# Performance work log

Hardware: AMD Instinct MI355X
Metric: run time of the kernel (lower is better)

Reference implementation:

```python
import jax, jax.numpy as jnp
import numpy as np

CONTACT_THRESH = 0.01
COLLISION_THRESH = 0.005
WEIGHT_PEN = 100.0
WEIGHT_MISS = 10.0
# MANO fingertip + palm contact-zone vertex indices (hardcoded in module)
CONTACT_IDX = np.array([745, 317, 444, 556, 673, 95, 182, 234, 279, 320])

SCALE = 0.1  # place points in a 0.1 m cube so mm-scale thresholds are meaningful


def setup_inputs() -> dict:
    key = jax.random.key(0)
    k1, k2, k3, k4 = jax.random.split(key, 4)
    B, NH, V = 8, 778, 40000
    hand_verts = jax.random.uniform(k1, (B, NH, 3), dtype=jnp.float32) * SCALE
    obj_verts = jax.random.uniform(k2, (B, V, 3), dtype=jnp.float32) * SCALE
    hand_faces = jax.random.randint(k3, (1538, 3), 0, NH, dtype=jnp.int64 if jax.config.read('jax_enable_x64') else jnp.int32)
    obj_faces = jax.random.randint(k4, (79996, 3), 0, V, dtype=jnp.int64 if jax.config.read('jax_enable_x64') else jnp.int32)
    return {"hand_verts": hand_verts, "obj_verts": obj_verts,
            "hand_faces": hand_faces, "obj_faces": obj_faces}


def _min_dists(a, b):
    """Brute-force 1-NN: min Euclidean distance from each point in a [B,N,3] to b [B,M,3] -> [B,N]."""
    a_sq = jnp.sum(a * a, axis=-1, keepdims=True)          # [B,N,1]
    b_sq = jnp.sum(b * b, axis=-1)                          # [B,M]
    ab = jnp.einsum('bnd,bmd->bnm', a, b)                   # [B,N,M]
    d2 = jnp.maximum(a_sq + b_sq[:, None, :] - 2.0 * ab, 0.0)
    return jnp.sqrt(jnp.min(d2, axis=2))                    # [B,N]


def _masked_mean(vals, mask):
    cnt = jnp.sum(mask)
    s = jnp.sum(jnp.where(mask, vals, 0.0))
    return jnp.where(cnt > 0, s / jnp.maximum(cnt, 1).astype(vals.dtype), jnp.zeros((), vals.dtype))


def reference(hand_verts, obj_verts, hand_faces, obj_faces):
    # faces are unused by the loss (as in the torch module)
    idx = jnp.asarray(CONTACT_IDX)
    # distances are computed under no_grad / detached in the original
    dists = jax.lax.stop_gradient(_min_dists(hand_verts, obj_verts))              # [B,778]
    contact_dists = jax.lax.stop_gradient(_min_dists(hand_verts[:, idx, :], obj_verts))  # [B,10]

    pen_mask = dists < COLLISION_THRESH
    pen_loss = _masked_mean((COLLISION_THRESH - dists) ** 2, pen_mask)

    att_mask = (contact_dists > COLLISION_THRESH) & (contact_dists < CONTACT_THRESH)
    att_loss = _masked_mean(contact_dists ** 2, att_mask)

    contact_loss = WEIGHT_PEN * pen_loss + WEIGHT_MISS * att_loss
    dist_mean = jnp.mean(dists)
    num_contacts = jnp.sum(att_mask).astype(jnp.int32)
    num_penetrations = jnp.sum(pen_mask).astype(jnp.int32)
    return (contact_loss, pen_loss, att_loss, dist_mean, num_contacts, num_penetrations)
```

## Files before the change

### kernel.cpp

```cpp
#include <hip/hip_runtime.h>
#include <math.h>

constexpr int NH    = 778;
constexpr int GRIDC = 16;
constexpr int NCELL = GRIDC * GRIDC * GRIDC;
constexpr int CAP   = 40;
constexpr float CELL     = 0.1f / GRIDC;
constexpr float INV_CELL = GRIDC / 0.1f;
constexpr int NXCD = 8;


__device__ __forceinline__ int clampc(int v) {
    return min(GRIDC - 1, max(0, v));
}

__global__ __launch_bounds__(256) void bin_kernel(
    const float* __restrict__ obj,
    int* __restrict__ cnt,
    int* __restrict__ ocnt,
    float4* __restrict__ buckets,
    float4* __restrict__ ovf,
    int B, int V, int bpb)
{
    const int w = (blockIdx.x % NXCD) * (gridDim.x / NXCD) + blockIdx.x / NXCD;
    const int b = w / bpb;
    const int p = (w % bpb) * 256 + threadIdx.x;
    if (b >= B || p >= V) return;
    const int i = b * V + p;

    const float x = obj[3 * i + 0];
    const float y = obj[3 * i + 1];
    const float z = obj[3 * i + 2];
    const int cx = clampc((int)(x * INV_CELL));
    const int cy = clampc((int)(y * INV_CELL));
    const int cz = clampc((int)(z * INV_CELL));
    const int cell = b * NCELL + (cz * GRIDC + cy) * GRIDC + cx;
    const int idx = atomicAdd(&cnt[cell], 1);
    if (idx < CAP) {
        buckets[(size_t)cell * CAP + idx] = make_float4(x, y, z, 0.f);
    } else {
        const int oi = atomicAdd(ocnt, 1);
        ovf[oi] = make_float4(x, y, z, __int_as_float(b));
    }
}

__global__ __launch_bounds__(256) void query_kernel(
    const float* __restrict__ hand,
    const int* __restrict__ cnt,
    const float4* __restrict__ buckets,
    const float4* __restrict__ ovf,
    const int* __restrict__ ocnt,
    float* __restrict__ dist,
    int B, int bpq)
{
    const int tid  = threadIdx.x;
    const int wave = tid >> 6;
    const int lane = tid & 63;
    const int w = (blockIdx.x % NXCD) * (gridDim.x / NXCD) + blockIdx.x / NXCD;
    const int b  = w / bpq;
    const int ql = (w % bpq) * 4 + wave;
    if (b >= B || ql >= NH) return;
    const int i = b * NH + ql;

    const float hx = hand[3 * i + 0];
    const float hy = hand[3 * i + 1];
    const float hz = hand[3 * i + 2];
    const int hcx = clampc((int)(hx * INV_CELL));
    const int hcy = clampc((int)(hy * INV_CELL));
    const int hcz = clampc((int)(hz * INV_CELL));
    const int cbase = b * NCELL;

    float best = 3.4e38f;

    if (lane < 54) {
        const int cl  = lane >> 1;
        const int sub = lane & 1;
        const int cx = hcx + (cl % 3) - 1;
        const int cy = hcy + ((cl / 3) % 3) - 1;
        const int cz = hcz + (cl / 9) - 1;
        if (cx >= 0 && cx < GRIDC && cy >= 0 && cy < GRIDC &&
            cz >= 0 && cz < GRIDC) {
            const int cell = cbase + (cz * GRIDC + cy) * GRIDC + cx;
            const int n = min(cnt[cell], CAP);
            const float4* bp = buckets + (size_t)cell * CAP;
            for (int k = sub; k < n; k += 2) {
                const float4 p = bp[k];
                const float dx = p.x - hx, dy = p.y - hy, dz = p.z - hz;
                best = fminf(best, fmaf(dx, dx, fmaf(dy, dy, dz * dz)));
            }
        }
    }

    const int on = *ocnt;
    for (int k = lane; k < on; k += 64) {
        const float4 p = ovf[k];
        if (__float_as_int(p.w) == b) {
            const float dx = p.x - hx, dy = p.y - hy, dz = p.z - hz;
            best = fminf(best, fmaf(dx, dx, fmaf(dy, dy, dz * dz)));
        }
    }

#pragma unroll
    for (int d = 1; d < 64; d <<= 1) best = fminf(best, __shfl_xor(best, d));

    for (int r = 2; r < GRIDC; ++r) {
        const float bnd = (float)(r - 1) * CELL;
        if (best <= bnd * bnd) break;
        const int side = 2 * r + 1;
        const int ncells = side * side * side;
        for (int ci = lane; ci < ncells; ci += 64) {
            const int dx = ci % side - r;
            const int dy = (ci / side) % side - r;
            const int dz = ci / (side * side) - r;
            if (max(max(abs(dx), abs(dy)), abs(dz)) != r) continue;
            const int cx = hcx + dx, cy = hcy + dy, cz = hcz + dz;
            if (cx < 0 || cx >= GRIDC || cy < 0 || cy >= GRIDC ||
                cz < 0 || cz >= GRIDC) continue;
            const int cell = cbase + (cz * GRIDC + cy) * GRIDC + cx;
            const int n = min(cnt[cell], CAP);
            const float4* bp = buckets + (size_t)cell * CAP;
            for (int k = 0; k < n; ++k) {
                const float4 p = bp[k];
                const float ddx = p.x - hx, ddy = p.y - hy, ddz = p.z - hz;
                best = fminf(best, fmaf(ddx, ddx, fmaf(ddy, ddy, ddz * ddz)));
            }
        }
#pragma unroll
        for (int d = 1; d < 64; d <<= 1) best = fminf(best, __shfl_xor(best, d));
    }

    if (lane == 0) dist[i] = best;
}

typedef float v2f __attribute__((ext_vector_type(2)));
constexpr int FT = 16, FG = 4, FBLK = 256, FCHUNK = 2560;
constexpr int FNBX = (NH + FG * FT - 1) / (FG * FT);
constexpr int FLPP = FCHUNK / FBLK, FPP = FLPP / 2;

__global__ __launch_bounds__(FBLK, 2) void nn_brute_kernel(
    const float* __restrict__ hand, const float* __restrict__ obj,
    unsigned int* __restrict__ minb, int V)
{
    __shared__ float s_red[4][16 * 65];
    const int bx = blockIdx.x, c = blockIdx.y, b = blockIdx.z;
    const int tid = threadIdx.x, wave = tid >> 6, lane = tid & 63;
    const int r = lane & 15, seg = lane >> 4;
    const float* ob = obj + (size_t)b * V * 3;
    const int base = c * FCHUNK + tid;
    v2f ox2[FPP], oy2[FPP], oz2[FPP], oq2[FPP];
#pragma unroll
    for (int p = 0; p < FPP; ++p) {
        const int ja = min(base + (2 * p + 0) * FBLK, V - 1);
        const int jb = min(base + (2 * p + 1) * FBLK, V - 1);
        const float xa = ob[3 * ja], ya = ob[3 * ja + 1], za = ob[3 * ja + 2];
        const float xb = ob[3 * jb], yb = ob[3 * jb + 1], zb = ob[3 * jb + 2];
        ox2[p] = (v2f){-2.f * xa, -2.f * xb};
        oy2[p] = (v2f){-2.f * ya, -2.f * yb};
        oz2[p] = (v2f){-2.f * za, -2.f * zb};
        oq2[p] = (v2f){fmaf(xa, xa, fmaf(ya, ya, za * za)),
                       fmaf(xb, xb, fmaf(yb, yb, zb * zb))};
    }
    const float* hb = hand + (size_t)b * NH * 3;
    float* sw = &s_red[wave][0];
#pragma unroll 1
    for (int g = 0; g < FG; ++g) {
        float hx[FT], hy[FT], hz[FT], m[FT];
#pragma unroll
        for (int t = 0; t < FT; ++t) {
            const int h = min((bx * FG + g) * FT + t, NH - 1);
            hx[t] = hb[3 * h]; hy[t] = hb[3 * h + 1]; hz[t] = hb[3 * h + 2];
            m[t] = 3.4e38f;
        }
#pragma unroll
        for (int p = 0; p < FPP; ++p) {
#pragma unroll
            for (int t = 0; t < FT; ++t) {
                v2f a = __builtin_elementwise_fma(ox2[p], (v2f){hx[t], hx[t]}, oq2[p]);
                a = __builtin_elementwise_fma(oy2[p], (v2f){hy[t], hy[t]}, a);
                a = __builtin_elementwise_fma(oz2[p], (v2f){hz[t], hz[t]}, a);
                m[t] = fminf(fminf(a.x, a.y), m[t]);
            }
        }
#pragma unroll
        for (int t = 0; t < FT; ++t) {
            const float hq = fmaf(hx[t], hx[t], fmaf(hy[t], hy[t], hz[t] * hz[t]));
            sw[t * 65 + lane] = m[t] + hq;
        }
        __builtin_amdgcn_wave_barrier();
        float v = 3.4e38f;
        const int rb = r * 65 + seg * 16;
#pragma unroll
        for (int j = 0; j < 16; ++j) v = fminf(v, sw[rb + j]);
        __builtin_amdgcn_wave_barrier();
        v = fminf(v, __shfl_xor(v, 16));
        v = fminf(v, __shfl_xor(v, 32));
        if (seg == 0) {
            const int hidx = (bx * FG + g) * FT + r;
            if (hidx < NH) {
                const unsigned bits = __float_as_uint(fmaxf(v, 0.f));
                unsigned int* p = &minb[b * NH + hidx];
                if (bits < *((volatile unsigned int*)p)) atomicMin(p, bits);
            }
        }
    }
}

__global__ __launch_bounds__(256) void finalize_kernel(
    const float* __restrict__ dist, float* __restrict__ out, int B)
{
    constexpr float COLL = 0.005f;
    constexpr float CONT = 0.01f;
    const int total = B * NH;
    const int tid = threadIdx.x;

    double sum_d = 0.0, pen_sum = 0.0, att_sum = 0.0;
    int pen_cnt = 0, att_cnt = 0;
    for (int i = tid; i < total; i += 256) {
        const float d = sqrtf(fmaxf(dist[i], 0.f));
        sum_d += (double)d;
        if (d < COLL) { const float t = COLL - d; pen_sum += (double)(t * t); pen_cnt++; }
        const int n = i % NH;
        const bool isc = (n == 745) | (n == 317) | (n == 444) | (n == 556) |
                         (n == 673) | (n == 95)  | (n == 182) | (n == 234) |
                         (n == 279) | (n == 320);
        if (isc & (d > COLL) & (d < CONT)) { att_sum += (double)(d * d); att_cnt++; }
    }

    __shared__ double sd[256], sp[256], sa[256];
    __shared__ int    cp[256], ca[256];
    sd[tid] = sum_d; sp[tid] = pen_sum; sa[tid] = att_sum;
    cp[tid] = pen_cnt; ca[tid] = att_cnt;
    __syncthreads();
    for (int off = 128; off > 0; off >>= 1) {
        if (tid < off) {
            sd[tid] += sd[tid + off]; sp[tid] += sp[tid + off];
            sa[tid] += sa[tid + off];
            cp[tid] += cp[tid + off]; ca[tid] += ca[tid + off];
        }
        __syncthreads();
    }
    if (tid == 0) {
        const double pen_loss = cp[0] > 0 ? sp[0] / (double)cp[0] : 0.0;
        const double att_loss = ca[0] > 0 ? sa[0] / (double)ca[0] : 0.0;
        out[0] = (float)(100.0 * pen_loss + 10.0 * att_loss);
        out[1] = (float)pen_loss;
        out[2] = (float)att_loss;
        out[3] = (float)(sd[0] / (double)total);
        out[4] = (float)ca[0];
        out[5] = (float)cp[0];
    }
}

extern "C" void kernel_launch(void* const* d_in, const int* in_sizes, int n_in,
                              void* d_out, int out_size, void* d_ws, size_t ws_size,
                              hipStream_t stream) {
    const float* hand = (const float*)d_in[0];
    const float* obj  = (const float*)d_in[1];

    const int B = in_sizes[0] / (NH * 3);
    const int V = in_sizes[1] / (B * 3);
    const int total = B * V;

    float* dist = (float*)d_ws;
    char* base = (char*)d_ws;
    size_t off = 65536;
    int* cnt = (int*)(base + off);
    const size_t cnt_bytes = (size_t)B * NCELL * sizeof(int);
    int* ocnt = (int*)(base + off + cnt_bytes);
    size_t boff = (off + cnt_bytes + 256) & ~(size_t)255;
    float4* buckets = (float4*)(base + boff);
    const size_t bkt_bytes = (size_t)B * NCELL * CAP * sizeof(float4);
    float4* ovf = (float4*)(base + boff + bkt_bytes);
    const size_t need = boff + bkt_bytes + (size_t)total * sizeof(float4);

    if (ws_size >= need) {
        hipMemsetAsync(cnt, 0, cnt_bytes + 64, stream);

        const int bpb = (V + 255) / 256;
        int gbin = B * bpb; gbin = (gbin + NXCD - 1) & ~(NXCD - 1);
        bin_kernel<<<gbin, 256, 0, stream>>>(obj, cnt, ocnt, buckets, ovf,
                                             B, V, bpb);

        const int bpq = (NH + 3) / 4;
        int gq = B * bpq; gq = (gq + NXCD - 1) & ~(NXCD - 1);
        query_kernel<<<gq, 256, 0, stream>>>(hand, cnt, buckets, ovf, ocnt,
                                             dist, B, bpq);
    } else {
        hipMemsetAsync(d_ws, 0x7F, (size_t)B * NH * sizeof(unsigned int), stream);
        dim3 grid(FNBX, (V + FCHUNK - 1) / FCHUNK, B);
        nn_brute_kernel<<<grid, FBLK, 0, stream>>>(hand, obj,
                                                   (unsigned int*)d_ws, V);
    }
    finalize_kernel<<<1, 256, 0, stream>>>(dist, (float*)d_out, B);
}
```

Baseline: 95.56 us.

## Fuse loss reduction into query kernel via sharded atomics and vectorize binning

The query kernel now computes per-vertex loss terms right away and accumulates block partial sums into 64 cache-line-padded shards with atomics. A tiny one-wave finalize kernel then replaces the 256-thread finalize pass over the distance array. The binning kernel handles 4 points per thread using three float4 loads, which cuts thread count and improves load width. The contact indices are now hardcoded as comparisons, and double atomics are added in exchange for removing the per-vertex distance buffer round-trip.

```diff
diff --git a/kernel.cpp b/kernel.cpp
--- a/kernel.cpp
+++ b/kernel.cpp
@@ -8,7 +8,14 @@
 constexpr float CELL     = 0.1f / GRIDC;
 constexpr float INV_CELL = GRIDC / 0.1f;
 constexpr int NXCD = 8;
-
+constexpr int NSH  = 64;
+
+
+struct alignas(64) Shard {
+    double sd, sp, sa;
+    int cp, ca;
+    int pad[3];
+};
 
 __device__ __forceinline__ int clampc(int v) {
     return min(GRIDC - 1, max(0, v));
@@ -24,23 +31,45 @@
 {
     const int w = (blockIdx.x % NXCD) * (gridDim.x / NXCD) + blockIdx.x / NXCD;
     const int b = w / bpb;
-    const int p = (w % bpb) * 256 + threadIdx.x;
-    if (b >= B || p >= V) return;
-    const int i = b * V + p;
-
-    const float x = obj[3 * i + 0];
-    const float y = obj[3 * i + 1];
-    const float z = obj[3 * i + 2];
-    const int cx = clampc((int)(x * INV_CELL));
-    const int cy = clampc((int)(y * INV_CELL));
-    const int cz = clampc((int)(z * INV_CELL));
-    const int cell = b * NCELL + (cz * GRIDC + cy) * GRIDC + cx;
-    const int idx = atomicAdd(&cnt[cell], 1);
-    if (idx < CAP) {
-        buckets[(size_t)cell * CAP + idx] = make_float4(x, y, z, 0.f);
+    if (b >= B) return;
+    const int p0 = ((w % bpb) * 256 + (int)threadIdx.x) * 4;
+    if (p0 >= V) return;
+
+    float px[4], py[4], pz[4];
+    int np;
+    const size_t fbase = ((size_t)b * V + p0) * 3;
+    if (p0 + 4 <= V && (fbase & 3) == 0) {
+        const float4* src = (const float4*)(obj + fbase);
+        const float4 A = src[0], Bv = src[1], C = src[2];
+        px[0]=A.x;  py[0]=A.y;  pz[0]=A.z;
+        px[1]=A.w;  py[1]=Bv.x; pz[1]=Bv.y;
+        px[2]=Bv.z; py[2]=Bv.w; pz[2]=C.x;
+        px[3]=C.y;  py[3]=C.z;  pz[3]=C.w;
+        np = 4;
     } else {
-        const int oi = atomicAdd(ocnt, 1);
-        ovf[oi] = make_float4(x, y, z, __int_as_float(b));
+        np = min(4, V - p0);
+        for (int q = 0; q < np; ++q) {
+            px[q] = obj[fbase + 3 * q + 0];
+            py[q] = obj[fbase + 3 * q + 1];
+            pz[q] = obj[fbase + 3 * q + 2];
+        }
+    }
+
+    const int cb = b * NCELL;
+#pragma unroll
+    for (int q = 0; q < 4; ++q) {
+        if (q >= np) break;
+        const int cx = clampc((int)(px[q] * INV_CELL));
+        const int cy = clampc((int)(py[q] * INV_CELL));
+        const int cz = clampc((int)(pz[q] * INV_CELL));
+        const int cell = cb + (cz * GRIDC + cy) * GRIDC + cx;
+        const int idx = atomicAdd(&cnt[cell], 1);
+        if (idx < CAP) {
+            buckets[(size_t)cell * CAP + idx] = make_float4(px[q], py[q], pz[q], 0.f);
+        } else {
+            const int oi = atomicAdd(ocnt, 1);
+            ovf[oi] = make_float4(px[q], py[q], pz[q], __int_as_float(b));
+        }
     }
 }
 
@@ -50,86 +79,146 @@
     const float4* __restrict__ buckets,
     const float4* __restrict__ ovf,
     const int* __restrict__ ocnt,
-    float* __restrict__ dist,
+    Shard* __restrict__ shards,
     int B, int bpq)
 {
+    constexpr float COLL = 0.005f;
+    constexpr float CONT = 0.01f;
     const int tid  = threadIdx.x;
     const int wave = tid >> 6;
     const int lane = tid & 63;
-    const int w = (blockIdx.x % NXCD) * (gridDim.x / NXCD) + blockIdx.x / NXCD;
+    const int w  = (blockIdx.x % NXCD) * (gridDim.x / NXCD) + blockIdx.x / NXCD;
     const int b  = w / bpq;
     const int ql = (w % bpq) * 4 + wave;
-    if (b >= B || ql >= NH) return;
-    const int i = b * NH + ql;
-
-    const float hx = hand[3 * i + 0];
-    const float hy = hand[3 * i + 1];
-    const float hz = hand[3 * i + 2];
-    const int hcx = clampc((int)(hx * INV_CELL));
-    const int hcy = clampc((int)(hy * INV_CELL));
-    const int hcz = clampc((int)(hz * INV_CELL));
-    const int cbase = b * NCELL;
+    const bool valid = (b < B) && (ql < NH);
 
     float best = 3.4e38f;
 
-    if (lane < 54) {
-        const int cl  = lane >> 1;
-        const int sub = lane & 1;
-        const int cx = hcx + (cl % 3) - 1;
-        const int cy = hcy + ((cl / 3) % 3) - 1;
-        const int cz = hcz + (cl / 9) - 1;
-        if (cx >= 0 && cx < GRIDC && cy >= 0 && cy < GRIDC &&
-            cz >= 0 && cz < GRIDC) {
-            const int cell = cbase + (cz * GRIDC + cy) * GRIDC + cx;
-            const int n = min(cnt[cell], CAP);
-            const float4* bp = buckets + (size_t)cell * CAP;
-            for (int k = sub; k < n; k += 2) {
-                const float4 p = bp[k];
+    if (valid) {
+        const int i = b * NH + ql;
+        const float hx = hand[3 * i + 0];
+        const float hy = hand[3 * i + 1];
+        const float hz = hand[3 * i + 2];
+        const int hcx = clampc((int)(hx * INV_CELL));
+        const int hcy = clampc((int)(hy * INV_CELL));
+        const int hcz = clampc((int)(hz * INV_CELL));
+        const int cbase = b * NCELL;
+
+        if (lane < 54) {
+            const int cl  = lane >> 1;
+            const int sub = lane & 1;
+            const int cx = hcx + (cl % 3) - 1;
+            const int cy = hcy + ((cl / 3) % 3) - 1;
+            const int cz = hcz + (cl / 9) - 1;
+            if (cx >= 0 && cx < GRIDC && cy >= 0 && cy < GRIDC &&
+                cz >= 0 && cz < GRIDC) {
+                const int cell = cbase + (cz * GRIDC + cy) * GRIDC + cx;
+                const int n = min(cnt[cell], CAP);
+                const float4* bp = buckets + (size_t)cell * CAP;
+                for (int k = sub; k < n; k += 2) {
+                    const float4 p = bp[k];
+                    const float dx = p.x - hx, dy = p.y - hy, dz = p.z - hz;
+                    best = fminf(best, fmaf(dx, dx, fmaf(dy, dy, dz * dz)));
+                }
+            }
+        }
+
+        const int on = *ocnt;
+        for (int k = lane; k < on; k += 64) {
+            const float4 p = ovf[k];
+            if (__float_as_int(p.w) == b) {
                 const float dx = p.x - hx, dy = p.y - hy, dz = p.z - hz;
                 best = fminf(best, fmaf(dx, dx, fmaf(dy, dy, dz * dz)));
             }
         }
-    }
-
-    const int on = *ocnt;
-    for (int k = lane; k < on; k += 64) {
-        const float4 p = ovf[k];
-        if (__float_as_int(p.w) == b) {
-            const float dx = p.x - hx, dy = p.y - hy, dz = p.z - hz;
-            best = fminf(best, fmaf(dx, dx, fmaf(dy, dy, dz * dz)));
-        }
-    }
-
-#pragma unroll
-    for (int d = 1; d < 64; d <<= 1) best = fminf(best, __shfl_xor(best, d));
-
-    for (int r = 2; r < GRIDC; ++r) {
-        const float bnd = (float)(r - 1) * CELL;
-        if (best <= bnd * bnd) break;
-        const int side = 2 * r + 1;
-        const int ncells = side * side * side;
-        for (int ci = lane; ci < ncells; ci += 64) {
-            const int dx = ci % side - r;
-            const int dy = (ci / side) % side - r;
-            const int dz = ci / (side * side) - r;
-            if (max(max(abs(dx), abs(dy)), abs(dz)) != r) continue;
-            const int cx = hcx + dx, cy = hcy + dy, cz = hcz + dz;
-            if (cx < 0 || cx >= GRIDC || cy < 0 || cy >= GRIDC ||
-                cz < 0 || cz >= GRIDC) continue;
-            const int cell = cbase + (cz * GRIDC + cy) * GRIDC + cx;
-            const int n = min(cnt[cell], CAP);
-            const float4* bp = buckets + (size_t)cell * CAP;
-            for (int k = 0; k < n; ++k) {
-                const float4 p = bp[k];
-                const float ddx = p.x - hx, ddy = p.y - hy, ddz = p.z - hz;
-                best = fminf(best, fmaf(ddx, ddx, fmaf(ddy, ddy, ddz * ddz)));
-            }
-        }
+
 #pragma unroll
         for (int d = 1; d < 64; d <<= 1) best = fminf(best, __shfl_xor(best, d));
-    }
-
-    if (lane == 0) dist[i] = best;
+
+        for (int r = 2; r < GRIDC; ++r) {
+            const float bnd = (float)(r - 1) * CELL;
+            if (best <= bnd * bnd) break;
+            const int side = 2 * r + 1;
+            const int ncells = side * side * side;
+            for (int ci = lane; ci < ncells; ci += 64) {
+                const int dx = ci % side - r;
+                const int dy = (ci / side) % side - r;
+                const int dz = ci / (side * side) - r;
+                if (max(max(abs(dx), abs(dy)), abs(dz)) != r) continue;
+                const int cx = hcx + dx, cy = hcy + dy, cz = hcz + dz;
+                if (cx < 0 || cx >= GRIDC || cy < 0 || cy >= GRIDC ||
+                    cz < 0 || cz >= GRIDC) continue;
+                const int cell = cbase + (cz * GRIDC + cy) * GRIDC + cx;
+                const int n = min(cnt[cell], CAP);
+                const float4* bp = buckets + (size_t)cell * CAP;
+                for (int k = 0; k < n; ++k) {
+                    const float4 p = bp[k];
+                    const float ddx = p.x - hx, ddy = p.y - hy, ddz = p.z - hz;
+                    best = fminf(best, fmaf(ddx, ddx, fmaf(ddy, ddy, ddz * ddz)));
+                }
+            }
+#pragma unroll
+            for (int d = 1; d < 64; d <<= 1) best = fminf(best, __shfl_xor(best, d));
+        }
+    }
+
+    __shared__ double ssd[4], ssp[4], ssa[4];
+    __shared__ int scp[4], sca[4];
+    if (lane == 0) {
+        double sd = 0.0, sp = 0.0, sa = 0.0;
+        int cp = 0, ca = 0;
+        if (valid) {
+            const float d = sqrtf(fmaxf(best, 0.f));
+            sd = (double)d;
+            if (d < COLL) { const float t = COLL - d; sp = (double)(t * t); cp = 1; }
+            const bool isc = (ql == 745) | (ql == 317) | (ql == 444) | (ql == 556) |
+                             (ql == 673) | (ql == 95)  | (ql == 182) | (ql == 234) |
+                             (ql == 279) | (ql == 320);
+            if (isc & (d > COLL) & (d < CONT)) { sa = (double)(d * d); ca = 1; }
+        }
+        ssd[wave] = sd; ssp[wave] = sp; ssa[wave] = sa;
+        scp[wave] = cp; sca[wave] = ca;
+    }
+    __syncthreads();
+    if (tid == 0) {
+        const double sd = ssd[0] + ssd[1] + ssd[2] + ssd[3];
+        const double sp = ssp[0] + ssp[1] + ssp[2] + ssp[3];
+        const double sa = ssa[0] + ssa[1] + ssa[2] + ssa[3];
+        const int cp = scp[0] + scp[1] + scp[2] + scp[3];
+        const int ca = sca[0] + sca[1] + sca[2] + sca[3];
+        Shard* s = &shards[blockIdx.x & (NSH - 1)];
+        atomicAdd(&s->sd, sd);
+        atomicAdd(&s->sp, sp);
+        atomicAdd(&s->sa, sa);
+        atomicAdd(&s->cp, cp);
+        atomicAdd(&s->ca, ca);
+    }
+}
+
+__global__ __launch_bounds__(64) void finalize_tiny(
+    const Shard* __restrict__ shards, float* __restrict__ out, int nq)
+{
+    const int l = threadIdx.x;
+    double sd = shards[l].sd, sp = shards[l].sp, sa = shards[l].sa;
+    int cp = shards[l].cp, ca = shards[l].ca;
+#pragma unroll
+    for (int d = 1; d < 64; d <<= 1) {
+        sd += __shfl_xor(sd, d);
+        sp += __shfl_xor(sp, d);
+        sa += __shfl_xor(sa, d);
+        cp += __shfl_xor(cp, d);
+        ca += __shfl_xor(ca, d);
+    }
+    if (l == 0) {
+        const double pen_loss = cp > 0 ? sp / (double)cp : 0.0;
+        const double att_loss = ca > 0 ? sa / (double)ca : 0.0;
+        out[0] = (float)(100.0 * pen_loss + 10.0 * att_loss);
+        out[1] = (float)pen_loss;
+        out[2] = (float)att_loss;
+        out[3] = (float)(sd / (double)nq);
+        out[4] = (float)ca;
+        out[5] = (float)cp;
+    }
 }
 
 typedef float v2f __attribute__((ext_vector_type(2)));
@@ -260,23 +349,24 @@
     const int B = in_sizes[0] / (NH * 3);
     const int V = in_sizes[1] / (B * 3);
     const int total = B * V;
-
-    float* dist = (float*)d_ws;
+    const int nq = B * NH;
+
     char* base = (char*)d_ws;
     size_t off = 65536;
-    int* cnt = (int*)(base + off);
+    Shard* shards = (Shard*)(base + off);
+    int*   ocnt   = (int*)(base + off + 4096);
+    int*   cnt    = (int*)(base + off + 8192);
     const size_t cnt_bytes = (size_t)B * NCELL * sizeof(int);
-    int* ocnt = (int*)(base + off + cnt_bytes);
-    size_t boff = (off + cnt_bytes + 256) & ~(size_t)255;
+    const size_t boff = (off + 8192 + cnt_bytes + 255) & ~(size_t)255;
     float4* buckets = (float4*)(base + boff);
     const size_t bkt_bytes = (size_t)B * NCELL * CAP * sizeof(float4);
     float4* ovf = (float4*)(base + boff + bkt_bytes);
     const size_t need = boff + bkt_bytes + (size_t)total * sizeof(float4);
 
     if (ws_size >= need) {
-        hipMemsetAsync(cnt, 0, cnt_bytes + 64, stream);
-
-        const int bpb = (V + 255) / 256;
+        hipMemsetAsync(base + off, 0, 8192 + cnt_bytes, stream);
+
+        const int bpb = (V + 1023) / 1024;
         int gbin = B * bpb; gbin = (gbin + NXCD - 1) & ~(NXCD - 1);
         bin_kernel<<<gbin, 256, 0, stream>>>(obj, cnt, ocnt, buckets, ovf,
                                              B, V, bpb);
@@ -284,12 +374,14 @@
         const int bpq = (NH + 3) / 4;
         int gq = B * bpq; gq = (gq + NXCD - 1) & ~(NXCD - 1);
         query_kernel<<<gq, 256, 0, stream>>>(hand, cnt, buckets, ovf, ocnt,
-                                             dist, B, bpq);
+                                             shards, B, bpq);
+
+        finalize_tiny<<<1, 64, 0, stream>>>(shards, (float*)d_out, nq);
     } else {
-        hipMemsetAsync(d_ws, 0x7F, (size_t)B * NH * sizeof(unsigned int), stream);
+        hipMemsetAsync(d_ws, 0x7F, (size_t)nq * sizeof(unsigned int), stream);
         dim3 grid(FNBX, (V + FCHUNK - 1) / FCHUNK, B);
         nn_brute_kernel<<<grid, FBLK, 0, stream>>>(hand, obj,
                                                    (unsigned int*)d_ws, V);
-    }
-    finalize_kernel<<<1, 256, 0, stream>>>(dist, (float*)d_out, B);
-}
+        finalize_kernel<<<1, 256, 0, stream>>>((const float*)d_ws, (float*)d_out, B);
+    }
+}
```

Result: faster. 88.43 us (-7.5%).
